# Performance work log

Hardware: AMD Instinct MI355X
Metric: run time of the kernel (lower is better)

## Reference

```python
import jax, jax.numpy as jnp
import numpy as np

BS, GRID, LSTM_H, CNN_C, PROJ = 256, 49, 512, 2048, 512


def setup_inputs() -> dict:
    key = jax.random.key(0)
    ks = jax.random.split(key, 7)
    s = lambda fan_in: 1.0 / np.sqrt(fan_in)
    return {
        "lstm_hidden": jax.random.normal(ks[0], (BS, LSTM_H), jnp.float32),
        "cnn_feat": jax.random.normal(ks[1], (BS, GRID, CNN_C), jnp.float32),
        "W_lstm": jax.random.normal(ks[2], (PROJ, LSTM_H), jnp.float32) * s(LSTM_H),
        "b_lstm": jax.random.normal(ks[3], (PROJ,), jnp.float32) * s(LSTM_H),
        "W_cnn": jax.random.normal(ks[4], (PROJ, CNN_C), jnp.float32) * s(CNN_C),
        "b_cnn": jax.random.normal(ks[5], (PROJ,), jnp.float32) * s(CNN_C),
        "w_attn": jax.random.normal(ks[6], (1, PROJ), jnp.float32) * s(PROJ),
    }


def reference(lstm_hidden, cnn_feat, W_lstm, b_lstm, W_cnn, b_cnn, w_attn):
    # H computed once (original loop recomputes it per grid, identically)
    H = lstm_hidden @ W_lstm.T + b_lstm                       # (bs, P)
    V = jnp.einsum("bgc,pc->bgp", cnn_feat, W_cnn) + b_cnn    # (bs, G, P)
    z = jnp.tanh(H[:, None, :] + V) @ w_attn[0]               # (bs, G)
    bs, G = z.shape
    # Faithful to torch: cat over grids along dim 0 -> (G*bs,), then view(bs, G)
    z_scrambled = jnp.swapaxes(z, 0, 1).reshape(bs, G)
    return jax.nn.softmax(z_scrambled, axis=1)
```

## Files before the change

### kernel.cpp

```cpp
#include <hip/hip_runtime.h>
#include <math.h>

#define BSZ    256
#define GRID_N 49
#define LSTMH  512
#define CNN_C  2048
#define PROJ   512
#define KAUG   2560
#define M_TOT  12544
#define BK     64
#define KTILES (KAUG / BK)

#define MT2    128
#define NT2    128
#define NBLK2  ((M_TOT / MT2) * (PROJ / NT2))

#define MT     64
#define NT     128
#define NBLK   ((M_TOT / MT) * (PROJ / NT))

#define WBLK   640

typedef short bf16x8 __attribute__((ext_vector_type(8)));
typedef float f32x4  __attribute__((ext_vector_type(4)));

static __device__ __forceinline__ unsigned short bf16_rne(float f) {
    unsigned int u = __float_as_uint(f);
    u = u + 0x7FFFu + ((u >> 16) & 1u);
    return (unsigned short)(u >> 16);
}
static __device__ __forceinline__ uint4 pack8f(const float* f) {
    uint4 o;
    o.x = (unsigned int)bf16_rne(f[0]) | ((unsigned int)bf16_rne(f[1]) << 16);
    o.y = (unsigned int)bf16_rne(f[2]) | ((unsigned int)bf16_rne(f[3]) << 16);
    o.z = (unsigned int)bf16_rne(f[4]) | ((unsigned int)bf16_rne(f[5]) << 16);
    o.w = (unsigned int)bf16_rne(f[6]) | ((unsigned int)bf16_rne(f[7]) << 16);
    return o;
}
static __device__ __forceinline__ float tanh_fast(float x) {
    float e = __expf(2.f * x);
    return 1.f - 2.f / (e + 1.f);
}
static __device__ __forceinline__ void glds16(const void* g, void* l) {
    __builtin_amdgcn_global_load_lds(
        (const __attribute__((address_space(1))) unsigned int*)g,
        (__attribute__((address_space(3))) unsigned int*)l, 16, 0, 0);
}

__global__ __launch_bounds__(256) void prep_w(const float* __restrict__ Wc,
                                              const float* __restrict__ Wl,
                                              unsigned short* __restrict__ wsW,
                                              float* __restrict__ out) {
    const int bid = blockIdx.x, t = threadIdx.x;
    if (bid < 49) out[bid * 256 + t] = 0.f;
    int c  = bid * 256 + t;
    int p  = c / 320;
    int kc = (c % 320) * 8;
    const float* src = (kc < CNN_C) ? (Wc + (size_t)p * CNN_C + kc)
                                    : (Wl + (size_t)p * LSTMH + (kc - CNN_C));
    float f[8];
    *(float4*)&f[0] = ((const float4*)src)[0];
    *(float4*)&f[4] = ((const float4*)src)[1];
    *(uint4*)(wsW + (size_t)p * KAUG + kc) = pack8f(f);
}

__global__ __launch_bounds__(256, 2) void gemm9(
    const float* __restrict__ lstm, const float* __restrict__ cnn,
    const unsigned short* __restrict__ wsW,
    const float* __restrict__ bl, const float* __restrict__ bc,
    const float* __restrict__ wat, float* __restrict__ out)
{
    __shared__ unsigned short Ab[2][MT2][BK];
    __shared__ unsigned short Bb[2][NT2][BK];

    const int t   = threadIdx.x;
    const int w   = t >> 6;
    const int l   = t & 63;
    const int q   = l >> 4;
    const int r16 = l & 15;
    const int wr  = w >> 1;
    const int wc  = w & 1;

    const int bid = (int)blockIdx.x;
    const int swz = (bid & 7) * (NBLK2 / 8) + (bid >> 3);
    const int m0  = (swz >> 2) * MT2;
    const int n0  = (swz & 3) * NT2;

    const int srow = l >> 3;
    const int cg   = (l & 7) ^ srow;

    const int ar  = t >> 1;
    const int ac0 = (t & 1) * 4;
    const int sw  = ar & 7;
    const int grow = m0 + ar;
    const int ab_  = grow / 49;
    const int ag_  = grow - ab_ * 49;
    const float* cnnb  = cnn + ((size_t)ab_ * GRID_N + ag_) * CNN_C;
    const float* lstmb = lstm + (size_t)ab_ * LSTMH;

    float4 fa[8];
    auto a_load = [&](int kt) {
        const int k0 = kt * BK;
        const float* s = (((k0 < CNN_C) ? (cnnb + k0) : (lstmb + (k0 - CNN_C)))) + ac0 * 8;
        #pragma unroll
        for (int i = 0; i < 8; ++i) fa[i] = ((const float4*)s)[i];
    };
    auto a_pack_write = [&](int bufi) {
        #pragma unroll
        for (int c = 0; c < 4; ++c) {
            const float4 x = fa[2 * c], y = fa[2 * c + 1];
            uint4 o;
            asm("v_cvt_pk_bf16_f32 %0, %1, %2" : "=v"(o.x) : "v"(x.x), "v"(x.y));
            asm("v_cvt_pk_bf16_f32 %0, %1, %2" : "=v"(o.y) : "v"(x.z), "v"(x.w));
            asm("v_cvt_pk_bf16_f32 %0, %1, %2" : "=v"(o.z) : "v"(y.x), "v"(y.y));
            asm("v_cvt_pk_bf16_f32 %0, %1, %2" : "=v"(o.w) : "v"(y.z), "v"(y.w));
            *(uint4*)&Ab[bufi][ar][((ac0 + c) ^ sw) * 8] = o;
        }
    };
    auto b_stage = [&](int kt, int bufi) {
        const int k0 = kt * BK;
        #pragma unroll
        for (int j = 0; j < 4; ++j) {
            const int rowb = w * 32 + j * 8;
            const unsigned short* g = wsW + (size_t)(n0 + rowb + srow) * KAUG + k0 + cg * 8;
            glds16(g, &Bb[bufi][rowb][0]);
        }
    };

    f32x4 acc[4][4];
    #pragma unroll
    for (int mt = 0; mt < 4; ++mt)
        #pragma unroll
        for (int nt = 0; nt < 4; ++nt)
            acc[mt][nt] = (f32x4){0.f, 0.f, 0.f, 0.f};

    a_load(0);
    b_stage(0, 0);
    a_pack_write(0);
    a_load(1);
    b_stage(1, 1);
    asm volatile("s_waitcnt lgkmcnt(0)" ::: "memory");

    for (int kt = 0; kt < KTILES; ++kt) {
        const int cur = kt & 1;
        if (kt + 1 < KTILES) {
            asm volatile("s_waitcnt vmcnt(12)" ::: "memory");
        } else {
            asm volatile("s_waitcnt vmcnt(0)" ::: "memory");
        }
        __builtin_amdgcn_s_barrier();
        if (kt + 1 < KTILES) a_pack_write(cur ^ 1);
        if (kt + 2 < KTILES) a_load(kt + 2);
        __builtin_amdgcn_sched_barrier(0);
        #pragma unroll
        for (int ks = 0; ks < 2; ++ks) {
            const int cp = ((ks * 4 + q) ^ (r16 & 7)) * 8;
            bf16x8 af[4], bfr[4];
            #pragma unroll
            for (int mt = 0; mt < 4; ++mt)
                af[mt] = *(const bf16x8*)&Ab[cur][wr * 64 + mt * 16 + r16][cp];
            #pragma unroll
            for (int nt = 0; nt < 4; ++nt)
                bfr[nt] = *(const bf16x8*)&Bb[cur][wc * 64 + nt * 16 + r16][cp];
            #pragma unroll
            for (int mt = 0; mt < 4; ++mt)
                #pragma unroll
                for (int nt = 0; nt < 4; ++nt)
                    acc[mt][nt] = __builtin_amdgcn_mfma_f32_16x16x32_bf16(
                        af[mt], bfr[nt], acc[mt][nt], 0, 0, 0);
        }
        asm volatile("s_waitcnt lgkmcnt(0)" ::: "memory");
        __builtin_amdgcn_s_barrier();
        if (kt + 2 < KTILES) b_stage(kt + 2, cur);
    }

    float* zpf = (float*)&Ab[0][0][0];
    float part[4][4];
    #pragma unroll
    for (int mt = 0; mt < 4; ++mt)
        #pragma unroll
        for (int rr = 0; rr < 4; ++rr) part[mt][rr] = 0.f;
    #pragma unroll
    for (int nt = 0; nt < 4; ++nt) {
        const int p = n0 + wc * 64 + nt * 16 + r16;
        const float bb = bl[p] + bc[p];
        const float wa = wat[p];
        #pragma unroll
        for (int mt = 0; mt < 4; ++mt)
            #pragma unroll
            for (int rr = 0; rr < 4; ++rr)
                part[mt][rr] += tanh_fast(acc[mt][nt][rr] + bb) * wa;
    }
    #pragma unroll
    for (int mt = 0; mt < 4; ++mt)
        #pragma unroll
        for (int rr = 0; rr < 4; ++rr) {
            float v = part[mt][rr];
            v += __shfl_xor(v, 1);
            v += __shfl_xor(v, 2);
            v += __shfl_xor(v, 4);
            v += __shfl_xor(v, 8);
            if (r16 == 0) zpf[wc * MT2 + wr * 64 + mt * 16 + q * 4 + rr] = v;
        }
    __syncthreads();
    if (t < MT2) {
        const float v = zpf[t] + zpf[MT2 + t];
        const int row = m0 + t;
        const int b2  = row / 49;
        const int g2  = row - b2 * 49;
        atomicAdd(&out[g2 * BSZ + b2], v);
    }
}

__global__ __launch_bounds__(256, 4) void gemm_k(
    const float* __restrict__ lstm, const float* __restrict__ cnn,
    const float* __restrict__ Wc,   const float* __restrict__ Wl,
    const float* __restrict__ bl,   const float* __restrict__ bc,
    const float* __restrict__ wat,  float* __restrict__ out)
{
    __shared__ unsigned short Ash[MT][BK];
    __shared__ unsigned short Bsh[NT][BK];
    __shared__ float zp[4][MT];

    const int t   = threadIdx.x;
    const int w   = t >> 6;
    const int l   = t & 63;
    const int q   = l >> 4;
    const int r16 = l & 15;

    const int bid = (int)blockIdx.x;
    const int swz = (bid & 7) * (NBLK / 8) + (bid >> 3);
    const int m0 = (swz >> 2) * MT;
    const int n0 = (swz & 3) * NT;

    const int ra  = t >> 2;
    const int ca0 = t & 3;
    const int sa  = ra & 7;
    const int grow = m0 + ra;
    const int ab   = grow / 49;
    const int ag   = grow - ab * 49;
    const float* cnnb  = cnn + ((size_t)ab * GRID_N + ag) * CNN_C;
    const float* lstmb = lstm + (size_t)ab * LSTMH;

    f32x4 acc[4][2];
    #pragma unroll
    for (int mt = 0; mt < 4; ++mt)
        #pragma unroll
        for (int nt = 0; nt < 2; ++nt)
            acc[mt][nt] = (f32x4){0.f, 0.f, 0.f, 0.f};

    float4 fa0, fa1, fa2, fa3;

    auto a_load = [&](int k0) {
        const float* s = (k0 < CNN_C) ? (cnnb + k0) : (lstmb + (k0 - CNN_C));
        const float4* p0 = (const float4*)(s + ca0 * 8);
        const float4* p1 = (const float4*)(s + (ca0 + 4) * 8);
        fa0 = p0[0]; fa1 = p0[1];
        fa2 = p1[0]; fa3 = p1[1];
    };
    auto a_write = [&]() {
        float f[8];
        *(float4*)&f[0] = fa0; *(float4*)&f[4] = fa1;
        *(uint4*)&Ash[ra][(ca0 ^ sa) * 8] = pack8f(f);
        *(float4*)&f[0] = fa2; *(float4*)&f[4] = fa3;
        *(uint4*)&Ash[ra][((ca0 + 4) ^ sa) * 8] = pack8f(f);
    };
    auto b_stage = [&](int k0) {
        const int rb = t >> 1;
        const int hb = t & 1;
        const float* s = (k0 < CNN_C) ? (Wc + (size_t)(n0 + rb) * CNN_C + k0)
                                      : (Wl + (size_t)(n0 + rb) * LSTMH + (k0 - CNN_C));
        const int sw = rb & 7;
        #pragma unroll
        for (int c = 0; c < 4; ++c) {
            const int cc = hb * 4 + c;
            float f[8];
            *(float4*)&f[0] = ((const float4*)(s + cc * 8))[0];
            *(float4*)&f[4] = ((const float4*)(s + cc * 8))[1];
            *(uint4*)&Bsh[rb][(cc ^ sw) * 8] = pack8f(f);
        }
    };

    a_load(0);
    a_write();
    b_stage(0);

    for (int kt = 0; kt < KTILES; ++kt) {
        __syncthreads();
        const bool more = (kt + 1 < KTILES);
        if (more) a_load((kt + 1) * BK);
        #pragma unroll
        for (int ks = 0; ks < 2; ++ks) {
            const int cp = ((ks * 4 + q) ^ (r16 & 7)) * 8;
            bf16x8 af[4], bfr[2];
            #pragma unroll
            for (int mt = 0; mt < 4; ++mt)
                af[mt] = *(const bf16x8*)&Ash[mt * 16 + r16][cp];
            #pragma unroll
            for (int nt = 0; nt < 2; ++nt)
                bfr[nt] = *(const bf16x8*)&Bsh[w * 32 + nt * 16 + r16][cp];
            #pragma unroll
            for (int mt = 0; mt < 4; ++mt)
                #pragma unroll
                for (int nt = 0; nt < 2; ++nt)
                    acc[mt][nt] = __builtin_amdgcn_mfma_f32_16x16x32_bf16(
                        af[mt], bfr[nt], acc[mt][nt], 0, 0, 0);
        }
        __syncthreads();
        if (more) { a_write(); b_stage((kt + 1) * BK); }
    }

    float part[4][4];
    #pragma unroll
    for (int mt = 0; mt < 4; ++mt)
        #pragma unroll
        for (int rr = 0; rr < 4; ++rr) part[mt][rr] = 0.f;
    #pragma unroll
    for (int nt = 0; nt < 2; ++nt) {
        const int p = n0 + w * 32 + nt * 16 + r16;
        const float bb = bl[p] + bc[p];
        const float wa = wat[p];
        #pragma unroll
        for (int mt = 0; mt < 4; ++mt)
            #pragma unroll
            for (int rr = 0; rr < 4; ++rr)
                part[mt][rr] += tanh_fast(acc[mt][nt][rr] + bb) * wa;
    }
    #pragma unroll
    for (int mt = 0; mt < 4; ++mt)
        #pragma unroll
        for (int rr = 0; rr < 4; ++rr) {
            float v = part[mt][rr];
            v += __shfl_xor(v, 1);
            v += __shfl_xor(v, 2);
            v += __shfl_xor(v, 4);
            v += __shfl_xor(v, 8);
            if (r16 == 0) zp[w][mt * 16 + q * 4 + rr] = v;
        }
    __syncthreads();
    if (t < MT) {
        const float v = zp[0][t] + zp[1][t] + zp[2][t] + zp[3][t];
        const int row = m0 + t;
        const int b2  = row / 49;
        const int g2  = row - b2 * 49;
        atomicAdd(&out[g2 * BSZ + b2], v);
    }
}

__global__ __launch_bounds__(64) void softmax_rows(float* __restrict__ out)
{
    const int i = blockIdx.x;
    const int j = threadIdx.x;
    float x = (j < GRID_N) ? out[i * GRID_N + j] : -1e30f;
    float m = x;
    #pragma unroll
    for (int off = 32; off > 0; off >>= 1) m = fmaxf(m, __shfl_xor(m, off));
    float e = (j < GRID_N) ? __expf(x - m) : 0.f;
    float s = e;
    #pragma unroll
    for (int off = 32; off > 0; off >>= 1) s += __shfl_xor(s, off);
    if (j < GRID_N) out[i * GRID_N + j] = e / s;
}

extern "C" void kernel_launch(void* const* d_in, const int* in_sizes, int n_in,
                              void* d_out, int out_size, void* d_ws, size_t ws_size,
                              hipStream_t stream)
{
    const float* lstm = (const float*)d_in[0];
    const float* cnn  = (const float*)d_in[1];
    const float* Wl   = (const float*)d_in[2];
    const float* bl   = (const float*)d_in[3];
    const float* Wc   = (const float*)d_in[4];
    const float* bc   = (const float*)d_in[5];
    const float* wat  = (const float*)d_in[6];
    float* out = (float*)d_out;

    const size_t szW = (size_t)PROJ * KAUG * sizeof(unsigned short);

    if (ws_size >= szW) {
        unsigned short* wsW = (unsigned short*)d_ws;
        prep_w<<<dim3(WBLK), dim3(256), 0, stream>>>(Wc, Wl, wsW, out);
        gemm9<<<dim3(NBLK2), dim3(256), 0, stream>>>(lstm, cnn, wsW, bl, bc, wat, out);
    } else {
        hipMemsetAsync(out, 0, (size_t)out_size * sizeof(float), stream);
        gemm_k<<<dim3(NBLK), dim3(256), 0, stream>>>(lstm, cnn, Wc, Wl, bl, bc, wat, out);
    }
    softmax_rows<<<dim3(BSZ), dim3(64), 0, stream>>>(out);
}
```

Baseline: 253.7 us.

## Stage fp32 A tiles directly to LDS and convert to bf16 at fragment load

Replaces the register-staged A path (global load, convert to bf16, LDS write) with direct global-to-LDS async copies of fp32 A data, and converts to bf16 when reading MFMA fragments. The K tile shrinks from 64 to 32 with a new XOR swizzle, and occupancy is raised to 3 blocks per CU. The aim is to free VGPRs and remove the per-tile register round trip so loads overlap compute better. The cost is twice as many K iterations and barriers, and the same A data is converted repeatedly by the several waves that read it.

```diff
diff --git a/kernel.cpp b/kernel.cpp
--- a/kernel.cpp
+++ b/kernel.cpp
@@ -8,8 +8,8 @@
 #define PROJ   512
 #define KAUG   2560
 #define M_TOT  12544
-#define BK     64
-#define KTILES (KAUG / BK)
+#define BK2    32
+#define KT2    (KAUG / BK2)
 
 #define MT2    128
 #define NT2    128
@@ -17,6 +17,8 @@
 
 #define MT     64
 #define NT     128
+#define BK     64
+#define KTILES (KAUG / BK)
 #define NBLK   ((M_TOT / MT) * (PROJ / NT))
 
 #define WBLK   640
@@ -64,14 +66,14 @@
     *(uint4*)(wsW + (size_t)p * KAUG + kc) = pack8f(f);
 }
 
-__global__ __launch_bounds__(256, 2) void gemm9(
+__global__ __launch_bounds__(256, 3) void gemm10(
     const float* __restrict__ lstm, const float* __restrict__ cnn,
     const unsigned short* __restrict__ wsW,
     const float* __restrict__ bl, const float* __restrict__ bc,
     const float* __restrict__ wat, float* __restrict__ out)
 {
-    __shared__ unsigned short Ab[2][MT2][BK];
-    __shared__ unsigned short Bb[2][NT2][BK];
+    __shared__ float          Ab[2][MT2][BK2];
+    __shared__ unsigned short Bb[2][NT2][BK2];
 
     const int t   = threadIdx.x;
     const int w   = t >> 6;
@@ -86,46 +88,53 @@
     const int m0  = (swz >> 2) * MT2;
     const int n0  = (swz & 3) * NT2;
 
-    const int srow = l >> 3;
-    const int cg   = (l & 7) ^ srow;
-
-    const int ar  = t >> 1;
-    const int ac0 = (t & 1) * 4;
-    const int sw  = ar & 7;
-    const int grow = m0 + ar;
-    const int ab_  = grow / 49;
-    const int ag_  = grow - ab_ * 49;
-    const float* cnnb  = cnn + ((size_t)ab_ * GRID_N + ag_) * CNN_C;
-    const float* lstmb = lstm + (size_t)ab_ * LSTMH;
-
-    float4 fa[8];
-    auto a_load = [&](int kt) {
-        const int k0 = kt * BK;
-        const float* s = (((k0 < CNN_C) ? (cnnb + k0) : (lstmb + (k0 - CNN_C)))) + ac0 * 8;
-        #pragma unroll
-        for (int i = 0; i < 8; ++i) fa[i] = ((const float4*)s)[i];
+    const int aro = l >> 3;
+    const int cga = (l & 7) ^ aro;
+    const int bro = l >> 2;
+    const int cgb = (l & 3) ^ ((l >> 4) & 3);
+
+    const float* srcA[4]; const float* srcL[4]; const unsigned short* srcB[2];
+    #pragma unroll
+    for (int j = 0; j < 4; ++j) {
+        const int grow = m0 + w * 32 + j * 8 + aro;
+        srcA[j] = cnn  + (size_t)grow * CNN_C + cga * 4;
+        srcL[j] = lstm + (size_t)(grow / 49) * LSTMH + cga * 4;
+    }
+    #pragma unroll
+    for (int j = 0; j < 2; ++j) {
+        const int rowb = n0 + w * 32 + j * 16 + bro;
+        srcB[j] = wsW + (size_t)rowb * KAUG + cgb * 8;
+    }
+
+    auto stage = [&](int kt, int bufi) {
+        const int k0 = kt * BK2;
+        #pragma unroll
+        for (int j = 0; j < 2; ++j)
+            glds16(srcB[j] + k0, &Bb[bufi][w * 32 + j * 16][0]);
+        if (kt < 64) {
+            #pragma unroll
+            for (int j = 0; j < 4; ++j)
+                glds16(srcA[j] + k0, &Ab[bufi][w * 32 + j * 8][0]);
+        } else {
+            const int k0l = k0 - CNN_C;
+            #pragma unroll
+            for (int j = 0; j < 4; ++j)
+                glds16(srcL[j] + k0l, &Ab[bufi][w * 32 + j * 8][0]);
+        }
     };
-    auto a_pack_write = [&](int bufi) {
-        #pragma unroll
-        for (int c = 0; c < 4; ++c) {
-            const float4 x = fa[2 * c], y = fa[2 * c + 1];
-            uint4 o;
-            asm("v_cvt_pk_bf16_f32 %0, %1, %2" : "=v"(o.x) : "v"(x.x), "v"(x.y));
-            asm("v_cvt_pk_bf16_f32 %0, %1, %2" : "=v"(o.y) : "v"(x.z), "v"(x.w));
-            asm("v_cvt_pk_bf16_f32 %0, %1, %2" : "=v"(o.z) : "v"(y.x), "v"(y.y));
-            asm("v_cvt_pk_bf16_f32 %0, %1, %2" : "=v"(o.w) : "v"(y.z), "v"(y.w));
-            *(uint4*)&Ab[bufi][ar][((ac0 + c) ^ sw) * 8] = o;
-        }
-    };
-    auto b_stage = [&](int kt, int bufi) {
-        const int k0 = kt * BK;
-        #pragma unroll
-        for (int j = 0; j < 4; ++j) {
-            const int rowb = w * 32 + j * 8;
-            const unsigned short* g = wsW + (size_t)(n0 + rowb + srow) * KAUG + k0 + cg * 8;
-            glds16(g, &Bb[bufi][rowb][0]);
-        }
-    };
+
+    int Ra[4], ca0[4], ca1[4], Rb_[4], cb[4];
+    #pragma unroll
+    for (int mt = 0; mt < 4; ++mt) {
+        Ra[mt]  = wr * 64 + mt * 16 + r16;
+        ca0[mt] = (2 * q)     ^ (Ra[mt] & 7);
+        ca1[mt] = (2 * q + 1) ^ (Ra[mt] & 7);
+    }
+    #pragma unroll
+    for (int nt = 0; nt < 4; ++nt) {
+        Rb_[nt] = wc * 64 + nt * 16 + r16;
+        cb[nt]  = q ^ ((Rb_[nt] >> 2) & 3);
+    }
 
     f32x4 acc[4][4];
     #pragma unroll
@@ -134,44 +143,41 @@
         for (int nt = 0; nt < 4; ++nt)
             acc[mt][nt] = (f32x4){0.f, 0.f, 0.f, 0.f};
 
-    a_load(0);
-    b_stage(0, 0);
-    a_pack_write(0);
-    a_load(1);
-    b_stage(1, 1);
-    asm volatile("s_waitcnt lgkmcnt(0)" ::: "memory");
-
-    for (int kt = 0; kt < KTILES; ++kt) {
+    stage(0, 0);
+    stage(1, 1);
+
+    for (int kt = 0; kt < KT2; ++kt) {
         const int cur = kt & 1;
-        if (kt + 1 < KTILES) {
-            asm volatile("s_waitcnt vmcnt(12)" ::: "memory");
+        if (kt + 1 < KT2) {
+            asm volatile("s_waitcnt vmcnt(6)" ::: "memory");
         } else {
             asm volatile("s_waitcnt vmcnt(0)" ::: "memory");
         }
         __builtin_amdgcn_s_barrier();
-        if (kt + 1 < KTILES) a_pack_write(cur ^ 1);
-        if (kt + 2 < KTILES) a_load(kt + 2);
-        __builtin_amdgcn_sched_barrier(0);
-        #pragma unroll
-        for (int ks = 0; ks < 2; ++ks) {
-            const int cp = ((ks * 4 + q) ^ (r16 & 7)) * 8;
-            bf16x8 af[4], bfr[4];
-            #pragma unroll
-            for (int mt = 0; mt < 4; ++mt)
-                af[mt] = *(const bf16x8*)&Ab[cur][wr * 64 + mt * 16 + r16][cp];
+        bf16x8 af[4], bfr[4];
+        #pragma unroll
+        for (int mt = 0; mt < 4; ++mt) {
+            const float* ar = &Ab[cur][Ra[mt]][0];
+            const float4 xa = *(const float4*)(ar + ca0[mt] * 4);
+            const float4 xb = *(const float4*)(ar + ca1[mt] * 4);
+            uint4 o;
+            asm("v_cvt_pk_bf16_f32 %0, %1, %2" : "=v"(o.x) : "v"(xa.x), "v"(xa.y));
+            asm("v_cvt_pk_bf16_f32 %0, %1, %2" : "=v"(o.y) : "v"(xa.z), "v"(xa.w));
+            asm("v_cvt_pk_bf16_f32 %0, %1, %2" : "=v"(o.z) : "v"(xb.x), "v"(xb.y));
+            asm("v_cvt_pk_bf16_f32 %0, %1, %2" : "=v"(o.w) : "v"(xb.z), "v"(xb.w));
+            af[mt] = *(bf16x8*)&o;
+        }
+        #pragma unroll
+        for (int nt = 0; nt < 4; ++nt)
+            bfr[nt] = *(const bf16x8*)&Bb[cur][Rb_[nt]][cb[nt] * 8];
+        #pragma unroll
+        for (int mt = 0; mt < 4; ++mt)
             #pragma unroll
             for (int nt = 0; nt < 4; ++nt)
-                bfr[nt] = *(const bf16x8*)&Bb[cur][wc * 64 + nt * 16 + r16][cp];
-            #pragma unroll
-            for (int mt = 0; mt < 4; ++mt)
-                #pragma unroll
-                for (int nt = 0; nt < 4; ++nt)
-                    acc[mt][nt] = __builtin_amdgcn_mfma_f32_16x16x32_bf16(
-                        af[mt], bfr[nt], acc[mt][nt], 0, 0, 0);
-        }
-        asm volatile("s_waitcnt lgkmcnt(0)" ::: "memory");
+                acc[mt][nt] = __builtin_amdgcn_mfma_f32_16x16x32_bf16(
+                    af[mt], bfr[nt], acc[mt][nt], 0, 0, 0);
         __builtin_amdgcn_s_barrier();
-        if (kt + 2 < KTILES) b_stage(kt + 2, cur);
+        if (kt + 2 < KT2) stage(kt + 2, cur);
     }
 
     float* zpf = (float*)&Ab[0][0][0];
@@ -380,7 +386,7 @@
     if (ws_size >= szW) {
         unsigned short* wsW = (unsigned short*)d_ws;
         prep_w<<<dim3(WBLK), dim3(256), 0, stream>>>(Wc, Wl, wsW, out);
-        gemm9<<<dim3(NBLK2), dim3(256), 0, stream>>>(lstm, cnn, wsW, bl, bc, wat, out);
+        gemm10<<<dim3(NBLK2), dim3(256), 0, stream>>>(lstm, cnn, wsW, bl, bc, wat, out);
     } else {
         hipMemsetAsync(out, 0, (size_t)out_size * sizeof(float), stream);
         gemm_k<<<dim3(NBLK), dim3(256), 0, stream>>>(lstm, cnn, Wc, Wl, bl, bc, wat, out);
```

Result: faster. 247.3 us (-2.5%).
